# Optimization experiments

Hardware: AMD Instinct MI355X
Metric: run time of the kernel (lower is better)

The kernel has to match this reference:

```python
import jax, jax.numpy as jnp
import numpy as np

N_TX = 50000; N_ADDR = 50000; E = 500000
IN = 128; C = 128; H = 4; D = 32  # C = hidden_channels = H*D
G = 512; OUT = 2
NEG_SLOPE = 0.2  # PyG HANConv default negative_slope


def _gat(h_src, h_dst, src, dst, a_src, a_dst, n_dst):
    # h_*: [N, H, D]; a_*: [H, D]; src/dst: [E]
    al_s = jnp.sum(h_src * a_src, axis=-1)  # [N_src, H]
    al_d = jnp.sum(h_dst * a_dst, axis=-1)  # [N_dst, H]
    alpha = jax.nn.leaky_relu(al_s[src] + al_d[dst], NEG_SLOPE)  # [E, H]
    # softmax over incoming edges of each destination node
    amax = jax.ops.segment_max(alpha, dst, num_segments=n_dst)
    ex = jnp.exp(alpha - amax[dst])
    denom = jax.ops.segment_sum(ex, dst, num_segments=n_dst)
    w = ex / (denom[dst] + 1e-16)  # PyG softmax adds 1e-16
    out = jax.ops.segment_sum(h_src[src] * w[:, :, None], dst, num_segments=n_dst)
    return jax.nn.relu(out.reshape(n_dst, H * D))


def _semantic(xs, q, Wk, bk):
    out = jnp.stack(xs)  # [K, N, C]
    score = jnp.sum(q * jnp.tanh(out @ Wk + bk).mean(axis=1), axis=-1)  # [K]
    attn = jax.nn.softmax(score)
    return jnp.sum(attn[:, None, None] * out, axis=0)  # [N, C]


def setup_inputs() -> dict:
    key = jax.random.key(0)
    k = jax.random.split(key, 24)
    s = 0.05
    return {
        "x_tx": jax.random.normal(k[0], (N_TX, IN), jnp.float32),
        "x_addr": jax.random.normal(k[1], (N_ADDR, IN), jnp.float32),
        "ei_ta": jnp.stack([jax.random.randint(k[2], (E,), 0, N_TX),
                            jax.random.randint(k[3], (E,), 0, N_ADDR)]),
        "ei_at": jnp.stack([jax.random.randint(k[4], (E,), 0, N_ADDR),
                            jax.random.randint(k[5], (E,), 0, N_TX)]),
        "ei_tt": jnp.stack([jax.random.randint(k[6], (E,), 0, N_TX),
                            jax.random.randint(k[7], (E,), 0, N_TX)]),
        "batch_tx": jnp.sort(jax.random.randint(k[8], (N_TX,), 0, G)),
        "W_tx": jax.random.normal(k[9], (IN, C), jnp.float32) / np.sqrt(IN).astype(np.float32),
        "b_tx": jnp.zeros((C,), jnp.float32),
        "W_addr": jax.random.normal(k[10], (IN, C), jnp.float32) / np.sqrt(IN).astype(np.float32),
        "b_addr": jnp.zeros((C,), jnp.float32),
        "a_src_ta": jax.random.normal(k[11], (H, D), jnp.float32) * s,
        "a_dst_ta": jax.random.normal(k[12], (H, D), jnp.float32) * s,
        "a_src_at": jax.random.normal(k[13], (H, D), jnp.float32) * s,
        "a_dst_at": jax.random.normal(k[14], (H, D), jnp.float32) * s,
        "a_src_tt": jax.random.normal(k[15], (H, D), jnp.float32) * s,
        "a_dst_tt": jax.random.normal(k[16], (H, D), jnp.float32) * s,
        "Wk": jax.random.normal(k[17], (C, C), jnp.float32) / np.sqrt(C).astype(np.float32),
        "bk": jnp.zeros((C,), jnp.float32),
        "q": jax.random.normal(k[18], (C,), jnp.float32) * s,
        "Wl": jax.random.normal(k[19], (C, OUT), jnp.float32) / np.sqrt(C).astype(np.float32),
        "bl": jnp.zeros((OUT,), jnp.float32),
    }


def reference(x_tx, x_addr, ei_ta, ei_at, ei_tt, batch_tx,
              W_tx, b_tx, W_addr, b_addr,
              a_src_ta, a_dst_ta, a_src_at, a_dst_at, a_src_tt, a_dst_tt,
              Wk, bk, q, Wl, bl):
    # per-node-type projection
    h_tx = (x_tx @ W_tx + b_tx).reshape(N_TX, H, D)
    h_ad = (x_addr @ W_addr + b_addr).reshape(N_ADDR, H, D)
    # per-edge-type GAT message passing (dropout disabled: eval mode)
    out_ta = _gat(h_tx, h_ad, ei_ta[0], ei_ta[1], a_src_ta, a_dst_ta, N_ADDR)
    out_at = _gat(h_ad, h_tx, ei_at[0], ei_at[1], a_src_at, a_dst_at, N_TX)
    out_tt = _gat(h_tx, h_tx, ei_tt[0], ei_tt[1], a_src_tt, a_dst_tt, N_TX)
    # semantic attention across metapaths ending at 'transaction'
    tx_feat = _semantic([out_at, out_tt], q, Wk, bk)  # [N_TX, C]
    # global_mean_pool over graph assignment
    sums = jax.ops.segment_sum(tx_feat, batch_tx, num_segments=G)
    cnts = jax.ops.segment_sum(jnp.ones((N_TX,), tx_feat.dtype), batch_tx, num_segments=G)
    pooled = sums / jnp.maximum(cnts, 1.0)[:, None]  # [G, C]
    return pooled @ Wl + bl  # [G, OUT]
```

## Files before the change

### kernel.cpp

```cpp
#include <hip/hip_runtime.h>

#define NTX   50000
#define NADDR 50000
#define NE    500000
#define GG    512
#define NEG   0.2f
#define MBLK  64
#define PBM   782
#define NCHUNK 196
#define GBLK  3125
#define EPB   640

typedef _Float16 f16;
typedef f16 f16x4 __attribute__((ext_vector_type(4)));
typedef f16 f16x8 __attribute__((ext_vector_type(8)));
typedef float f32x2 __attribute__((ext_vector_type(2)));
typedef float f32x4 __attribute__((ext_vector_type(4)));

__device__ __forceinline__ float lrelu(float x) { return x > 0.f ? x : NEG * x; }

__global__ __launch_bounds__(256) void prep_kernel(
    const float* __restrict__ W_tx, const float* __restrict__ W_ad,
    const float* __restrict__ Wk,
    f16* __restrict__ Wt_tx, f16* __restrict__ Wt_ad, f16* __restrict__ Wkt)
{
    const float* W = (blockIdx.y == 0) ? W_tx : (blockIdx.y == 1) ? W_ad : Wk;
    f16* Wt        = (blockIdx.y == 0) ? Wt_tx : (blockIdx.y == 1) ? Wt_ad : Wkt;
    __shared__ f16 tile[32][136];
    const int t = threadIdx.x;
    const int j0 = blockIdx.x * 32;
    for (int i = t; i < 32 * 128; i += 256) {
        int r = i >> 7, c = i & 127;
        tile[r][c] = (f16)W[(size_t)(j0 + r) * 128 + c];
    }
    __syncthreads();
    for (int i = t; i < 128 * 8; i += 256) {
        int c = i >> 3, q = i & 7;
        f16x4 p = { tile[q * 4 + 0][c], tile[q * 4 + 1][c],
                    tile[q * 4 + 2][c], tile[q * 4 + 3][c] };
        *(f16x4*)&Wt[(size_t)c * 128 + j0 + q * 4] = p;
    }
}

__global__ __launch_bounds__(256) void proj2_kernel(
    const float* __restrict__ x_tx, const f16* __restrict__ Wt_txg,
    const float* __restrict__ b_tx, f16* __restrict__ h_tx,
    const float* __restrict__ x_ad, const f16* __restrict__ Wt_adg,
    const float* __restrict__ b_ad, f16* __restrict__ h_ad,
    const float* __restrict__ a_dat, float* __restrict__ al_dat,
    const float* __restrict__ a_stt, float* __restrict__ al_stt,
    const float* __restrict__ a_dtt, float* __restrict__ al_dtt,
    const float* __restrict__ a_sat, float* __restrict__ al_sat,
    const int* __restrict__ ei0, const int* __restrict__ ei1,
    int* __restrict__ deg0, int* __restrict__ deg1,
    int* __restrict__ rank0, int* __restrict__ rank1)
{
    __shared__ f16 Wt[128][136];
    __shared__ f16 xt[MBLK][136];
    const bool is_tx = blockIdx.x < PBM;
    const float* x  = is_tx ? x_tx : x_ad;
    const f16* Wtg  = is_tx ? Wt_txg : Wt_adg;
    const float* b  = is_tx ? b_tx : b_ad;
    f16* h          = is_tx ? h_tx : h_ad;
    const int row0 = (is_tx ? blockIdx.x : blockIdx.x - PBM) * MBLK;
    const int t = threadIdx.x;

    {
        const f16x8* G = (const f16x8*)Wtg;
        for (int i = t; i < 128 * 16; i += 256) {
            int r = i >> 4, q = i & 15;
            *(f16x8*)&Wt[r][q * 8] = G[i];
        }
    }
    for (int i = t; i < MBLK * 32; i += 256) {
        int r = i >> 5, q = i & 31;
        int gr = row0 + r; if (gr >= NTX) gr = NTX - 1;
        float4 v = ((const float4*)x)[(size_t)gr * 32 + q];
        f16x4 p = {(f16)v.x, (f16)v.y, (f16)v.z, (f16)v.w};
        *(f16x4*)&xt[r][q * 4] = p;
    }
    __syncthreads();

    const int l = t & 63, w = t >> 6;
    const int l15 = l & 15, lq = l >> 4;

    f16x8 afrag[4];
#pragma unroll
    for (int kt = 0; kt < 4; kt++)
        afrag[kt] = *(const f16x8*)&xt[w * 16 + l15][kt * 32 + lq * 8];

    f32x4 acc[8];
#pragma unroll
    for (int n = 0; n < 8; n++) {
        float bc = b[n * 16 + l15];
        acc[n] = (f32x4){bc, bc, bc, bc};
#pragma unroll
        for (int kt = 0; kt < 4; kt++) {
            f16x8 bfrag = *(const f16x8*)&Wt[n * 16 + l15][kt * 32 + lq * 8];
            acc[n] = __builtin_amdgcn_mfma_f32_16x16x32_f16(afrag[kt], bfrag, acc[n], 0, 0, 0);
        }
    }

#pragma unroll
    for (int r = 0; r < 4; r++) {
        int row = row0 + w * 16 + lq * 4 + r;
        if (row < NTX) {
#pragma unroll
            for (int n = 0; n < 8; n++)
                h[(size_t)row * 128 + n * 16 + l15] = (f16)acc[n][r];
        }
    }

    auto do_dot = [&](const float* __restrict__ a, float* __restrict__ al) {
        float av[8];
#pragma unroll
        for (int n = 0; n < 8; n++) av[n] = a[n * 16 + l15];
#pragma unroll
        for (int r = 0; r < 4; r++) {
            float p0 = acc[0][r] * av[0] + acc[1][r] * av[1];
            float p1 = acc[2][r] * av[2] + acc[3][r] * av[3];
            float p2 = acc[4][r] * av[4] + acc[5][r] * av[5];
            float p3 = acc[6][r] * av[6] + acc[7][r] * av[7];
#pragma unroll
            for (int o = 1; o < 16; o <<= 1) {
                p0 += __shfl_xor(p0, o); p1 += __shfl_xor(p1, o);
                p2 += __shfl_xor(p2, o); p3 += __shfl_xor(p3, o);
            }
            int row = row0 + w * 16 + lq * 4 + r;
            if (l15 == 0 && row < NTX) {
                float4 v = make_float4(p0, p1, p2, p3);
                *(float4*)&al[(size_t)row * 4] = v;
            }
        }
    };
    if (is_tx) { do_dot(a_dat, al_dat); do_dot(a_stt, al_stt); do_dot(a_dtt, al_dtt); }
    else       { do_dot(a_sat, al_sat); }

    {
        const int e0 = blockIdx.x * EPB;
        const int e1 = min(e0 + EPB, 2 * NE);
        for (int e = e0 + t; e < e1; e += 256) {
            if (e < NE) {
                int d = ei0[NE + e];
                rank0[e] = atomicAdd(&deg0[d], 1);
            } else {
                int ee = e - NE;
                int d = ei1[NE + ee];
                rank1[ee] = atomicAdd(&deg1[d], 1);
            }
        }
    }
}

__global__ __launch_bounds__(256) void chunksum_kernel(
    const int* __restrict__ deg0, const int* __restrict__ deg1,
    int* __restrict__ csum)
{
    const int* deg = blockIdx.y == 0 ? deg0 : deg1;
    __shared__ int s[256];
    const int t = threadIdx.x;
    int idx = blockIdx.x * 256 + t;
    s[t] = idx < NTX ? deg[idx] : 0;
    __syncthreads();
    for (int o = 128; o > 0; o >>= 1) {
        if (t < o) s[t] += s[t + o];
        __syncthreads();
    }
    if (t == 0) csum[blockIdx.y * NCHUNK + blockIdx.x] = s[0];
}

__global__ __launch_bounds__(256) void chunkscan_kernel(int* __restrict__ csum)
{
    __shared__ int s[256];
    const int t = threadIdx.x;
    int* base = csum + blockIdx.x * NCHUNK;
    int v = t < NCHUNK ? base[t] : 0;
    s[t] = v;
    __syncthreads();
    for (int o = 1; o < 256; o <<= 1) {
        int u = (t >= o) ? s[t - o] : 0;
        __syncthreads();
        s[t] += u;
        __syncthreads();
    }
    if (t < NCHUNK) base[t] = s[t] - v;
}

__global__ __launch_bounds__(256) void scanwrite_kernel(
    const int* __restrict__ deg0, const int* __restrict__ deg1,
    const int* __restrict__ csum,
    int* __restrict__ row0, int* __restrict__ row1)
{
    const int* deg = blockIdx.y == 0 ? deg0 : deg1;
    int* row       = blockIdx.y == 0 ? row0 : row1;
    __shared__ int s[256];
    const int t = threadIdx.x;
    int idx = blockIdx.x * 256 + t;
    int v = idx < NTX ? deg[idx] : 0;
    s[t] = v;
    __syncthreads();
    for (int o = 1; o < 256; o <<= 1) {
        int u = (t >= o) ? s[t - o] : 0;
        __syncthreads();
        s[t] += u;
        __syncthreads();
    }
    if (idx < NTX)
        row[idx] = s[t] - v + csum[blockIdx.y * NCHUNK + blockIdx.x];
}

__global__ __launch_bounds__(256) void fill2_kernel(
    const int* __restrict__ ei0, const int* __restrict__ rank0,
    const int* __restrict__ row0, int* __restrict__ csr0,
    const int* __restrict__ ei1, const int* __restrict__ rank1,
    const int* __restrict__ row1, int* __restrict__ csr1)
{
    int idx = blockIdx.x * 256 + threadIdx.x;
    const int* ei; const int* rank; const int* row; int* csr;
    int e;
    if (idx < NE)          { ei = ei0; rank = rank0; row = row0; csr = csr0; e = idx; }
    else if (idx < 2 * NE) { ei = ei1; rank = rank1; row = row1; csr = csr1; e = idx - NE; }
    else return;
    int s = ei[e];
    int d = ei[NE + e];
    csr[row[d] + rank[e]] = s;
}

__global__ __launch_bounds__(256) void gat_gather2_kernel(
    const int* __restrict__ row_at, const int* __restrict__ deg_at,
    const int* __restrict__ csr_at, const float* __restrict__ als_at,
    const float* __restrict__ ald_at, const f16* __restrict__ h_at,
    f16* __restrict__ out_at,
    const int* __restrict__ row_tt, const int* __restrict__ deg_tt,
    const int* __restrict__ csr_tt, const float* __restrict__ als_tt,
    const float* __restrict__ ald_tt, const f16* __restrict__ h_tt,
    f16* __restrict__ out_tt)
{
    const int bid = blockIdx.x;
    const bool at = ((bid & 4) == 0);
    const int dblk = (bid >> 3) * 4 + (bid & 3);
    if (dblk >= GBLK) return;

    const int* rs = at ? row_at : row_tt;
    const int* dg = at ? deg_at : deg_tt;
    const int* cs = at ? csr_at : csr_tt;
    const float* als = at ? als_at : als_tt;
    const float* ald = at ? ald_at : ald_tt;
    const f16* hsrc = at ? h_at : h_tt;
    f16* out = at ? out_at : out_tt;

    const int t = threadIdx.x;
    const int d = dblk * 16 + (t >> 4);
    const int ln8 = t & 15;
    const int head = ln8 >> 2;
    const int beg = rs[d];
    const int n = dg[d];
    const float aldv = ald[d * 4 + head];
    const f16x8* H = (const f16x8*)hsrc;

    f32x2 acc[4] = {{0.f, 0.f}, {0.f, 0.f}, {0.f, 0.f}, {0.f, 0.f}};
    float den = 0.f;
    int i = 0;
    for (; i + 4 <= n; i += 4) {
        int s0 = cs[beg + i],     s1 = cs[beg + i + 1];
        int s2 = cs[beg + i + 2], s3 = cs[beg + i + 3];
        float l0 = als[s0 * 4 + head], l1 = als[s1 * 4 + head];
        float l2 = als[s2 * 4 + head], l3 = als[s3 * 4 + head];
        f16x8 h0 = H[(size_t)s0 * 16 + ln8];
        f16x8 h1 = H[(size_t)s1 * 16 + ln8];
        f16x8 h2 = H[(size_t)s2 * 16 + ln8];
        f16x8 h3 = H[(size_t)s3 * 16 + ln8];
        float w0 = __expf(lrelu(l0 + aldv));
        float w1 = __expf(lrelu(l1 + aldv));
        float w2 = __expf(lrelu(l2 + aldv));
        float w3 = __expf(lrelu(l3 + aldv));
        den += (w0 + w1) + (w2 + w3);
#pragma unroll
        for (int q = 0; q < 4; q++) {
            f32x2 a0 = {(float)h0[2 * q], (float)h0[2 * q + 1]};
            f32x2 a1 = {(float)h1[2 * q], (float)h1[2 * q + 1]};
            f32x2 a2 = {(float)h2[2 * q], (float)h2[2 * q + 1]};
            f32x2 a3 = {(float)h3[2 * q], (float)h3[2 * q + 1]};
            acc[q] = a0 * w0 + (a1 * w1 + (a2 * w2 + (a3 * w3 + acc[q])));
        }
    }
    for (; i < n; i++) {
        int s0 = cs[beg + i];
        float l0 = als[s0 * 4 + head];
        f16x8 h0 = H[(size_t)s0 * 16 + ln8];
        float w0 = __expf(lrelu(l0 + aldv));
        den += w0;
#pragma unroll
        for (int q = 0; q < 4; q++) {
            f32x2 a0 = {(float)h0[2 * q], (float)h0[2 * q + 1]};
            acc[q] = a0 * w0 + acc[q];
        }
    }
    float inv = 1.f / (den + 1e-16f);
    f16x8 o;
#pragma unroll
    for (int q = 0; q < 4; q++) {
        float v0 = acc[q][0] * inv, v1 = acc[q][1] * inv;
        o[2 * q]     = (f16)(v0 > 0.f ? v0 : 0.f);
        o[2 * q + 1] = (f16)(v1 > 0.f ? v1 : 0.f);
    }
    ((f16x8*)out)[(size_t)d * 16 + ln8] = o;
}

__global__ __launch_bounds__(256) void tanh_gemm_kernel(
    const f16* __restrict__ out_at, const f16* __restrict__ out_tt,
    const f16* __restrict__ Wktg, const float* __restrict__ bk,
    float* __restrict__ part)
{
    __shared__ f16 Wt[128][136];
    __shared__ f16 xt[MBLK][136];
    const int row0 = blockIdx.x * MBLK;
    const int t = threadIdx.x;

    {
        const f16x8* G = (const f16x8*)Wktg;
        for (int i = t; i < 128 * 16; i += 256) {
            int r = i >> 4, q = i & 15;
            *(f16x8*)&Wt[r][q * 8] = G[i];
        }
    }

    const int l = t & 63, w = t >> 6;
    const int l15 = l & 15, lq = l >> 4;

    for (int y = 0; y < 2; y++) {
        const f16* src = (y == 0) ? out_at : out_tt;
        __syncthreads();
        for (int i = t; i < MBLK * 16; i += 256) {
            int r = i >> 4, q = i & 15;
            int gr = row0 + r; if (gr >= NTX) gr = NTX - 1;
            *(f16x8*)&xt[r][q * 8] = ((const f16x8*)src)[(size_t)gr * 16 + q];
        }
        __syncthreads();

        f16x8 afrag[4];
#pragma unroll
        for (int kt = 0; kt < 4; kt++)
            afrag[kt] = *(const f16x8*)&xt[w * 16 + l15][kt * 32 + lq * 8];

        float pn[8];
#pragma unroll
        for (int n = 0; n < 8; n++) {
            float bc = bk[n * 16 + l15];
            f32x4 acc = (f32x4){bc, bc, bc, bc};
#pragma unroll
            for (int kt = 0; kt < 4; kt++) {
                f16x8 bfrag = *(const f16x8*)&Wt[n * 16 + l15][kt * 32 + lq * 8];
                acc = __builtin_amdgcn_mfma_f32_16x16x32_f16(afrag[kt], bfrag, acc, 0, 0, 0);
            }
            float s = 0.f;
#pragma unroll
            for (int r = 0; r < 4; r++) {
                int row = row0 + w * 16 + lq * 4 + r;
                if (row < NTX) s += tanhf(acc[r]);
            }
            s += __shfl_xor(s, 16);
            s += __shfl_xor(s, 32);
            pn[n] = s;
        }

        __syncthreads();
        float* Sblk = (float*)&xt[0][0];
        if (l < 16) {
#pragma unroll
            for (int n = 0; n < 8; n++)
                Sblk[w * 128 + n * 16 + l15] = pn[n];
        }
        __syncthreads();
        if (t < 128)
            part[((size_t)y * PBM + blockIdx.x) * 128 + t] =
                Sblk[t] + Sblk[128 + t] + Sblk[256 + t] + Sblk[384 + t];
    }
}

__global__ __launch_bounds__(128) void reduceS_kernel(
    const float* __restrict__ part, float* __restrict__ S_at, float* __restrict__ S_tt)
{
    const int k = blockIdx.y;
    const int c = threadIdx.x;
    float* S = (k == 0) ? S_at : S_tt;
    const int b0 = blockIdx.x * 25;
    const int b1 = min(b0 + 25, PBM);
    float s = 0.f;
    for (int b = b0; b < b1; b++)
        s += part[((size_t)k * PBM + b) * 128 + c];
    atomicAdd(&S[c], s);
}

__global__ __launch_bounds__(128) void attn_kernel(
    const float* __restrict__ S0, const float* __restrict__ S1,
    const float* __restrict__ q, float* __restrict__ attn)
{
    __shared__ float r0[128], r1[128];
    int c = threadIdx.x;
    r0[c] = q[c] * S0[c];
    r1[c] = q[c] * S1[c];
    __syncthreads();
    for (int s = 64; s > 0; s >>= 1) {
        if (c < s) { r0[c] += r0[c + s]; r1[c] += r1[c + s]; }
        __syncthreads();
    }
    if (c == 0) {
        float s0 = r0[0] / (float)NTX, s1 = r1[0] / (float)NTX;
        float m = fmaxf(s0, s1);
        float e0 = expf(s0 - m), e1 = expf(s1 - m);
        float inv = 1.f / (e0 + e1);
        attn[0] = e0 * inv;
        attn[1] = e1 * inv;
    }
}

__device__ __forceinline__ int lower_bound_g(const int* __restrict__ batch, int val)
{
    int lo = 0, hi = NTX;
    while (lo < hi) {
        int mid = (lo + hi) >> 1;
        if (batch[mid] < val) lo = mid + 1; else hi = mid;
    }
    return lo;
}

__global__ __launch_bounds__(1024) void final_pool_kernel(
    const f16* __restrict__ out_at, const f16* __restrict__ out_tt,
    const int* __restrict__ batch, const float* __restrict__ attn,
    const float* __restrict__ Wl, const float* __restrict__ bl,
    float* __restrict__ out)
{
    __shared__ float r0s[8][128], r1s[8][128];
    const int g = blockIdx.x;
    const int t = threadIdx.x;
    const int sub = t >> 7, c = t & 127;
    const int lo = lower_bound_g(batch, g);
    const int hi = lower_bound_g(batch, g + 1);
    float s0 = 0.f, s1 = 0.f;
    for (int n = lo + sub; n < hi; n += 8) {
        s0 += (float)out_at[(size_t)n * 128 + c];
        s1 += (float)out_tt[(size_t)n * 128 + c];
    }
    r0s[sub][c] = s0;
    r1s[sub][c] = s1;
    __syncthreads();
    for (int o = 4; o > 0; o >>= 1) {
        if (sub < o) {
            r0s[sub][c] += r0s[sub + o][c];
            r1s[sub][c] += r1s[sub + o][c];
        }
        __syncthreads();
    }
    if (t < 128) {
        float pooled = (attn[0] * r0s[0][t] + attn[1] * r1s[0][t])
                     / fmaxf((float)(hi - lo), 1.f);
        r0s[1][t] = pooled * Wl[t * 2 + 0];
        r1s[1][t] = pooled * Wl[t * 2 + 1];
    }
    __syncthreads();
    for (int s = 64; s > 0; s >>= 1) {
        if (t < s) { r0s[1][t] += r0s[1][t + s]; r1s[1][t] += r1s[1][t + s]; }
        __syncthreads();
    }
    if (t == 0) {
        out[g * 2 + 0] = r0s[1][0] + bl[0];
        out[g * 2 + 1] = r1s[1][0] + bl[1];
    }
}

extern "C" void kernel_launch(void* const* d_in, const int* in_sizes, int n_in,
                              void* d_out, int out_size, void* d_ws, size_t ws_size,
                              hipStream_t stream)
{
    const float* x_tx     = (const float*)d_in[0];
    const float* x_ad     = (const float*)d_in[1];
    const int*   ei_at    = (const int*)d_in[3];
    const int*   ei_tt    = (const int*)d_in[4];
    const int*   batch    = (const int*)d_in[5];
    const float* W_tx     = (const float*)d_in[6];
    const float* b_tx     = (const float*)d_in[7];
    const float* W_ad     = (const float*)d_in[8];
    const float* b_ad     = (const float*)d_in[9];
    const float* a_src_at = (const float*)d_in[12];
    const float* a_dst_at = (const float*)d_in[13];
    const float* a_src_tt = (const float*)d_in[14];
    const float* a_dst_tt = (const float*)d_in[15];
    const float* Wk       = (const float*)d_in[16];
    const float* bk       = (const float*)d_in[17];
    const float* q        = (const float*)d_in[18];
    const float* Wl       = (const float*)d_in[19];
    const float* bl       = (const float*)d_in[20];
    float* out = (float*)d_out;

    char* ws = (char*)d_ws;
    size_t off = 0;
    auto alloc = [&](size_t bytes) -> void* {
        void* p = ws + off;
        off += (bytes + 255) & ~(size_t)255;
        return p;
    };
    f16* h_tx      = (f16*)alloc((size_t)NTX * 128 * 2);
    f16* h_ad      = (f16*)alloc((size_t)NADDR * 128 * 2);
    f16* Wt_txg    = (f16*)alloc((size_t)128 * 128 * 2);
    f16* Wt_adg    = (f16*)alloc((size_t)128 * 128 * 2);
    f16* Wktg      = (f16*)alloc((size_t)128 * 128 * 2);
    float* al_sat  = (float*)alloc((size_t)NADDR * 4 * 4);
    float* al_dat  = (float*)alloc((size_t)NTX * 4 * 4);
    float* al_stt  = (float*)alloc((size_t)NTX * 4 * 4);
    float* al_dtt  = (float*)alloc((size_t)NTX * 4 * 4);
    f16* out_at    = (f16*)alloc((size_t)NTX * 128 * 2);
    f16* out_tt    = (f16*)alloc((size_t)NTX * 128 * 2);
    int* csr_at    = (int*)alloc((size_t)NE * 4);
    int* csr_tt    = (int*)alloc((size_t)NE * 4);
    int* rank_at   = (int*)alloc((size_t)NE * 4);
    int* rank_tt   = (int*)alloc((size_t)NE * 4);
    int* row_at    = (int*)alloc((size_t)NTX * 4);
    int* row_tt    = (int*)alloc((size_t)NTX * 4);
    int* csum      = (int*)alloc((size_t)2 * NCHUNK * 4);
    float* part    = (float*)alloc((size_t)2 * PBM * 128 * 4);
    char* zero0 = ws + off;
    int* deg_at    = (int*)alloc((size_t)NTX * 4);
    int* deg_tt    = (int*)alloc((size_t)NTX * 4);
    float* S_at    = (float*)alloc(128 * 4);
    float* S_tt    = (float*)alloc(128 * 4);
    size_t zbytes = (size_t)((ws + off) - zero0);
    float* attnw   = (float*)alloc(2 * 4);

    hipMemsetAsync(zero0, 0, zbytes, stream);

    dim3 pgrid(4, 3);
    prep_kernel<<<pgrid, 256, 0, stream>>>(W_tx, W_ad, Wk, Wt_txg, Wt_adg, Wktg);

    proj2_kernel<<<2 * PBM, 256, 0, stream>>>(
        x_tx, Wt_txg, b_tx, h_tx, x_ad, Wt_adg, b_ad, h_ad,
        a_dst_at, al_dat, a_src_tt, al_stt, a_dst_tt, al_dtt,
        a_src_at, al_sat,
        ei_at, ei_tt, deg_at, deg_tt, rank_at, rank_tt);

    dim3 sgrid(NCHUNK, 2);
    chunksum_kernel<<<sgrid, 256, 0, stream>>>(deg_at, deg_tt, csum);
    chunkscan_kernel<<<2, 256, 0, stream>>>(csum);
    scanwrite_kernel<<<sgrid, 256, 0, stream>>>(deg_at, deg_tt, csum, row_at, row_tt);
    int eb2 = (2 * NE + 255) / 256;
    fill2_kernel<<<eb2, 256, 0, stream>>>(
        ei_at, rank_at, row_at, csr_at,
        ei_tt, rank_tt, row_tt, csr_tt);

    gat_gather2_kernel<<<PBM * 8, 256, 0, stream>>>(
        row_at, deg_at, csr_at, al_sat, al_dat, h_ad, out_at,
        row_tt, deg_tt, csr_tt, al_stt, al_dtt, h_tx, out_tt);

    tanh_gemm_kernel<<<PBM, 256, 0, stream>>>(out_at, out_tt, Wktg, bk, part);
    dim3 rgrid(32, 2);
    reduceS_kernel<<<rgrid, 128, 0, stream>>>(part, S_at, S_tt);
    attn_kernel<<<1, 128, 0, stream>>>(S_at, S_tt, q, attnw);

    final_pool_kernel<<<GG, 1024, 0, stream>>>(out_at, out_tt, batch, attnw, Wl, bl, out);
}
```

Measured before the change: 190.8 us.

## Split degree counters into four sub-histograms and move edge counting earlier

The per-destination degree atomics are spread over four interleaved counter copies selected by edge index, which should cut contention on the same address. The counting loop also moves ahead of the MFMA projection work so its atomic latency can overlap with compute. Scan kernels now sum the four copies and emit per-copy base offsets so fill can place edges, plus a summed degree array for the gather. This costs extra memory traffic in the scan and fill passes, larger zeroed buffers, and more work before the first barrier.

```diff
diff --git a/kernel.cpp b/kernel.cpp
--- a/kernel.cpp
+++ b/kernel.cpp
@@ -79,6 +79,21 @@
         f16x4 p = {(f16)v.x, (f16)v.y, (f16)v.z, (f16)v.w};
         *(f16x4*)&xt[r][q * 4] = p;
     }
+
+    {
+        const int e0 = blockIdx.x * EPB;
+        const int e1 = min(e0 + EPB, 2 * NE);
+        for (int e = e0 + t; e < e1; e += 256) {
+            if (e < NE) {
+                int d = ei0[NE + e];
+                rank0[e] = atomicAdd(&deg0[(e & 3) * NTX + d], 1);
+            } else {
+                int ee = e - NE;
+                int d = ei1[NE + ee];
+                rank1[ee] = atomicAdd(&deg1[(ee & 3) * NTX + d], 1);
+            }
+        }
+    }
     __syncthreads();
 
     const int l = t & 63, w = t >> 6;
@@ -135,21 +150,6 @@
     };
     if (is_tx) { do_dot(a_dat, al_dat); do_dot(a_stt, al_stt); do_dot(a_dtt, al_dtt); }
     else       { do_dot(a_sat, al_sat); }
-
-    {
-        const int e0 = blockIdx.x * EPB;
-        const int e1 = min(e0 + EPB, 2 * NE);
-        for (int e = e0 + t; e < e1; e += 256) {
-            if (e < NE) {
-                int d = ei0[NE + e];
-                rank0[e] = atomicAdd(&deg0[d], 1);
-            } else {
-                int ee = e - NE;
-                int d = ei1[NE + ee];
-                rank1[ee] = atomicAdd(&deg1[d], 1);
-            }
-        }
-    }
 }
 
 __global__ __launch_bounds__(256) void chunksum_kernel(
@@ -160,7 +160,10 @@
     __shared__ int s[256];
     const int t = threadIdx.x;
     int idx = blockIdx.x * 256 + t;
-    s[t] = idx < NTX ? deg[idx] : 0;
+    int v = 0;
+    if (idx < NTX)
+        v = deg[idx] + deg[NTX + idx] + deg[2 * NTX + idx] + deg[3 * NTX + idx];
+    s[t] = v;
     __syncthreads();
     for (int o = 128; o > 0; o >>= 1) {
         if (t < o) s[t] += s[t + o];
@@ -189,14 +192,25 @@
 __global__ __launch_bounds__(256) void scanwrite_kernel(
     const int* __restrict__ deg0, const int* __restrict__ deg1,
     const int* __restrict__ csum,
-    int* __restrict__ row0, int* __restrict__ row1)
+    int* __restrict__ row0, int* __restrict__ row1,
+    int* __restrict__ degs0, int* __restrict__ degs1,
+    int* __restrict__ base0, int* __restrict__ base1)
 {
     const int* deg = blockIdx.y == 0 ? deg0 : deg1;
     int* row       = blockIdx.y == 0 ? row0 : row1;
+    int* degs      = blockIdx.y == 0 ? degs0 : degs1;
+    int* base      = blockIdx.y == 0 ? base0 : base1;
     __shared__ int s[256];
     const int t = threadIdx.x;
     int idx = blockIdx.x * 256 + t;
-    int v = idx < NTX ? deg[idx] : 0;
+    int d0 = 0, d1 = 0, d2 = 0, d3 = 0, v = 0;
+    if (idx < NTX) {
+        d0 = deg[idx];
+        d1 = deg[NTX + idx];
+        d2 = deg[2 * NTX + idx];
+        d3 = deg[3 * NTX + idx];
+        v = d0 + d1 + d2 + d3;
+    }
     s[t] = v;
     __syncthreads();
     for (int o = 1; o < 256; o <<= 1) {
@@ -205,25 +219,32 @@
         s[t] += u;
         __syncthreads();
     }
-    if (idx < NTX)
-        row[idx] = s[t] - v + csum[blockIdx.y * NCHUNK + blockIdx.x];
+    if (idx < NTX) {
+        int r = s[t] - v + csum[blockIdx.y * NCHUNK + blockIdx.x];
+        row[idx] = r;
+        degs[idx] = v;
+        base[idx]           = r;
+        base[NTX + idx]     = r + d0;
+        base[2 * NTX + idx] = r + d0 + d1;
+        base[3 * NTX + idx] = r + d0 + d1 + d2;
+    }
 }
 
 __global__ __launch_bounds__(256) void fill2_kernel(
     const int* __restrict__ ei0, const int* __restrict__ rank0,
-    const int* __restrict__ row0, int* __restrict__ csr0,
+    const int* __restrict__ base0, int* __restrict__ csr0,
     const int* __restrict__ ei1, const int* __restrict__ rank1,
-    const int* __restrict__ row1, int* __restrict__ csr1)
+    const int* __restrict__ base1, int* __restrict__ csr1)
 {
     int idx = blockIdx.x * 256 + threadIdx.x;
-    const int* ei; const int* rank; const int* row; int* csr;
+    const int* ei; const int* rank; const int* base; int* csr;
     int e;
-    if (idx < NE)          { ei = ei0; rank = rank0; row = row0; csr = csr0; e = idx; }
-    else if (idx < 2 * NE) { ei = ei1; rank = rank1; row = row1; csr = csr1; e = idx - NE; }
+    if (idx < NE)          { ei = ei0; rank = rank0; base = base0; csr = csr0; e = idx; }
+    else if (idx < 2 * NE) { ei = ei1; rank = rank1; base = base1; csr = csr1; e = idx - NE; }
     else return;
     int s = ei[e];
     int d = ei[NE + e];
-    csr[row[d] + rank[e]] = s;
+    csr[base[(e & 3) * NTX + d] + rank[e]] = s;
 }
 
 __global__ __launch_bounds__(256) void gat_gather2_kernel(
@@ -517,11 +538,15 @@
     int* rank_tt   = (int*)alloc((size_t)NE * 4);
     int* row_at    = (int*)alloc((size_t)NTX * 4);
     int* row_tt    = (int*)alloc((size_t)NTX * 4);
+    int* degs_at   = (int*)alloc((size_t)NTX * 4);
+    int* degs_tt   = (int*)alloc((size_t)NTX * 4);
+    int* base_at   = (int*)alloc((size_t)4 * NTX * 4);
+    int* base_tt   = (int*)alloc((size_t)4 * NTX * 4);
     int* csum      = (int*)alloc((size_t)2 * NCHUNK * 4);
     float* part    = (float*)alloc((size_t)2 * PBM * 128 * 4);
     char* zero0 = ws + off;
-    int* deg_at    = (int*)alloc((size_t)NTX * 4);
-    int* deg_tt    = (int*)alloc((size_t)NTX * 4);
+    int* deg_at    = (int*)alloc((size_t)4 * NTX * 4);
+    int* deg_tt    = (int*)alloc((size_t)4 * NTX * 4);
     float* S_at    = (float*)alloc(128 * 4);
     float* S_tt    = (float*)alloc(128 * 4);
     size_t zbytes = (size_t)((ws + off) - zero0);
@@ -541,15 +566,18 @@
     dim3 sgrid(NCHUNK, 2);
     chunksum_kernel<<<sgrid, 256, 0, stream>>>(deg_at, deg_tt, csum);
     chunkscan_kernel<<<2, 256, 0, stream>>>(csum);
-    scanwrite_kernel<<<sgrid, 256, 0, stream>>>(deg_at, deg_tt, csum, row_at, row_tt);
+    scanwrite_kernel<<<sgrid, 256, 0, stream>>>(deg_at, deg_tt, csum,
+                                                row_at, row_tt,
+                                                degs_at, degs_tt,
+                                                base_at, base_tt);
     int eb2 = (2 * NE + 255) / 256;
     fill2_kernel<<<eb2, 256, 0, stream>>>(
-        ei_at, rank_at, row_at, csr_at,
-        ei_tt, rank_tt, row_tt, csr_tt);
+        ei_at, rank_at, base_at, csr_at,
+        ei_tt, rank_tt, base_tt, csr_tt);
 
     gat_gather2_kernel<<<PBM * 8, 256, 0, stream>>>(
-        row_at, deg_at, csr_at, al_sat, al_dat, h_ad, out_at,
-        row_tt, deg_tt, csr_tt, al_stt, al_dtt, h_tx, out_tt);
+        row_at, degs_at, csr_at, al_sat, al_dat, h_ad, out_at,
+        row_tt, degs_tt, csr_tt, al_stt, al_dtt, h_tx, out_tt);
 
     tanh_gemm_kernel<<<PBM, 256, 0, stream>>>(out_at, out_tt, Wktg, bk, part);
     dim3 rgrid(32, 2);
```

Result: faster. 185.8 us (-2.7%).
